# Optimization experiments

Hardware: AMD Instinct MI355X
Metric: run time of the kernel (lower is better)

Reference implementation:

```python
import jax, jax.numpy as jnp
import numpy as np

B, N = 4, 8192


def _nn_idx(a, b):
    # For each point in a [B,Na,3], index of nearest point in b [B,Nb,3].
    # ||a-b||^2 = ||a||^2 - 2 a.b + ||b||^2 ; ||a||^2 is constant per row -> drop it.
    d = jnp.sum(b * b, axis=-1)[:, None, :] - 2.0 * jnp.einsum('bnd,bmd->bnm', a, b)
    return jnp.argmin(d, axis=-1)  # [B, Na]


def _thickness(white, pial):
    # Mirrors compute_thickness_vector: white = inner, pial = outer.
    bix = jnp.arange(white.shape[0])[:, None]
    i1 = _nn_idx(white, pial)            # NN in pial for each white point
    inner_th = pial[bix, i1] - white     # [B, Nw, 3]
    i2 = _nn_idx(pial, white)            # NN in white for each pial point
    outer_th = pial - white[bix, i2]     # [B, Np, 3]
    return inner_th, outer_th


def _msn(a, b):
    # MeanSquaredNormLoss with w=None: mean over all points of sum((a-b)^2, -1)
    return jnp.mean(jnp.sum((a - b) ** 2, axis=-1))


def _sym(a, b, i_a, i_b):
    # SymmetricMeanSquaredNormLoss.forward (batch_size > 1 path, no weights)
    bix = jnp.arange(a.shape[0])[:, None]
    return 0.5 * (_msn(a, b[bix, i_a]) + _msn(a[bix, i_b], b))


def setup_inputs() -> dict:
    key = jax.random.key(0)
    ks = jax.random.split(key, 8)
    return {
        'pred_white': jax.random.normal(ks[0], (B, N, 3), jnp.float32),
        'pred_pial': jax.random.normal(ks[1], (B, N, 3), jnp.float32),
        'true_white': jax.random.normal(ks[2], (B, N, 3), jnp.float32),
        'true_pial': jax.random.normal(ks[3], (B, N, 3), jnp.float32),
        'i_pred_white': jax.random.randint(ks[4], (B, N), 0, N, jnp.int32),
        'i_true_white': jax.random.randint(ks[5], (B, N), 0, N, jnp.int32),
        'i_pred_pial': jax.random.randint(ks[6], (B, N), 0, N, jnp.int32),
        'i_true_pial': jax.random.randint(ks[7], (B, N), 0, N, jnp.int32),
    }


def reference(pred_white, pred_pial, true_white, true_pial,
              i_pred_white, i_true_white, i_pred_pial, i_true_pial):
    yp_inner, yp_outer = _thickness(pred_white, pred_pial)
    yt_inner, yt_outer = _thickness(true_white, true_pial)
    return (0.5 * _sym(yp_inner, yt_inner, i_pred_white, i_true_white)
            + 0.5 * _sym(yp_outer, yt_outer, i_pred_pial, i_true_pial))
```

## Files before the change

### kernel.cpp

```cpp
#include <hip/hip_runtime.h>
#include <math.h>

#define BATCH 4
#define NPTS 8192
#define BN (BATCH * NPTS)
#define NDIR 4
#define NZB (NDIR * BATCH)

#define QK 8
#define SPL 8
#define SLICE (NPTS / SPL)
#define SUBT 128
#define NSUB (SLICE / SUBT)
#define NSUB_TOT (NPTS / SUBT)


__device__ __forceinline__ void pick_ab(int z, const float* pw, const float* pp,
                                        const float* tw, const float* tp,
                                        const float** qa, const float** cb) {
  if (z == 0)      { *qa = pw; *cb = pp; }
  else if (z == 1) { *qa = pp; *cb = pw; }
  else if (z == 2) { *qa = tw; *cb = tp; }
  else             { *qa = tp; *cb = tw; }
}

__global__ __launch_bounds__(256) void nn_partial_kernel(
    const float* __restrict__ pw, const float* __restrict__ pp,
    const float* __restrict__ tw, const float* __restrict__ tp,
    float* __restrict__ part_d, int* __restrict__ part_t,
    double* __restrict__ acc) {
  __shared__ float4 sh[SLICE];

  const int zb = blockIdx.z;
  const int z = zb >> 2;
  const int b = zb & 3;
  const float* qa;
  const float* cb;
  pick_ab(z, pw, pp, tw, tp, &qa, &cb);

  const int tid = threadIdx.x;
  const int cslice = blockIdx.y * SLICE;
  const float* cbb = cb + (size_t)b * NPTS * 3;

  for (int m = tid; m < SLICE; m += 256) {
    const float* c = cbb + (size_t)(cslice + m) * 3;
    const float bx = c[0], by = c[1], bz = c[2];
    sh[m] = make_float4(bx, by, bz, fmaf(bx, bx, fmaf(by, by, bz * bz)));
  }
  if (tid == 0 && blockIdx.x == 0 && blockIdx.y == 0 && blockIdx.z == 0)
    *acc = 0.0;
  __syncthreads();

  const int qbase = blockIdx.x * (256 * QK);
  float qx[QK], qy[QK], qz[QK], dmin[QK];
  int tile[QK];
  #pragma unroll
  for (int k = 0; k < QK; ++k) {
    const int n = qbase + tid + k * 256;
    const float* q = qa + ((size_t)b * NPTS + n) * 3;
    qx[k] = -2.0f * q[0];
    qy[k] = -2.0f * q[1];
    qz[k] = -2.0f * q[2];
    dmin[k] = INFINITY;
    tile[k] = 0;
  }

  for (int sub = 0; sub < NSUB; ++sub) {
    float pre[QK];
    #pragma unroll
    for (int k = 0; k < QK; ++k) pre[k] = dmin[k];

    const int base = sub * SUBT;
    #pragma unroll 2
    for (int m = 0; m < SUBT; ++m) {
      const float4 c = sh[base + m];
      #pragma unroll
      for (int k = 0; k < QK; ++k) {
        const float d = fmaf(qx[k], c.x, fmaf(qy[k], c.y, fmaf(qz[k], c.z, c.w)));
        dmin[k] = fminf(dmin[k], d);
      }
    }
    const int g = blockIdx.y * NSUB + sub;
    #pragma unroll
    for (int k = 0; k < QK; ++k)
      if (dmin[k] < pre[k]) tile[k] = g;
  }

  #pragma unroll
  for (int k = 0; k < QK; ++k) {
    const int n = qbase + tid + k * 256;
    const size_t o = ((size_t)zb * NPTS + n) * SPL + blockIdx.y;
    part_d[o] = dmin[k];
    part_t[o] = tile[k];
  }
}

__global__ __launch_bounds__(256) void nn_resolve_kernel(
    const float* __restrict__ pw, const float* __restrict__ pp,
    const float* __restrict__ tw, const float* __restrict__ tp,
    const float* __restrict__ part_d, const int* __restrict__ part_t,
    int* __restrict__ idx_all) {
  const int gid = blockIdx.x * 256 + threadIdx.x;
  const int zb = gid >> 13;
  const int n = gid & (NPTS - 1);
  const int z = zb >> 2;
  const int b = zb & 3;
  const float* qa;
  const float* cb;
  pick_ab(z, pw, pp, tw, tp, &qa, &cb);

  const size_t o = (size_t)gid * SPL;
  float best_d = part_d[o];
  int best_t = part_t[o];
  #pragma unroll
  for (int s = 1; s < SPL; ++s) {
    const float d = part_d[o + s];
    if (d < best_d) { best_d = d; best_t = part_t[o + s]; }
  }

  const float* q = qa + ((size_t)b * NPTS + n) * 3;
  const float qx = -2.0f * q[0];
  const float qy = -2.0f * q[1];
  const float qz = -2.0f * q[2];
  const float* cbb = cb + (size_t)b * NPTS * 3;
  const int m0 = best_t * SUBT;

  int best_i = NPTS;
  #pragma unroll 4
  for (int m = 0; m < SUBT; ++m) {
    const float* c = cbb + (size_t)(m0 + m) * 3;
    const float bx = c[0], by = c[1], bz = c[2];
    const float b2 = fmaf(bx, bx, fmaf(by, by, bz * bz));
    const float d = fmaf(qx, bx, fmaf(qy, by, fmaf(qz, bz, b2)));
    if (d == best_d && (m0 + m) < best_i) best_i = m0 + m;
  }
  idx_all[gid] = best_i;
}

__device__ __forceinline__ float3 ld3(const float* __restrict__ p, int i) {
  const float* q = p + (size_t)i * 3;
  return make_float3(q[0], q[1], q[2]);
}

__device__ __forceinline__ float diff_nrm2(float3 a1, float3 a2, float3 b1, float3 b2) {
  const float x = (a1.x - a2.x) - (b1.x - b2.x);
  const float y = (a1.y - a2.y) - (b1.y - b2.y);
  const float z = (a1.z - a2.z) - (b1.z - b2.z);
  return fmaf(x, x, fmaf(y, y, z * z));
}

__global__ __launch_bounds__(256) void loss_kernel(
    const float* __restrict__ pw, const float* __restrict__ pp,
    const float* __restrict__ tw, const float* __restrict__ tp,
    const int* __restrict__ ipw, const int* __restrict__ itw,
    const int* __restrict__ ipp, const int* __restrict__ itp,
    const int* __restrict__ idx_all, double* __restrict__ acc) {
  const int gid = blockIdx.x * 256 + threadIdx.x;
  const int term = blockIdx.y;
  const int b = gid >> 13;
  const int n = gid & (NPTS - 1);
  const int base = b * NPTS;

  const float* PW = pw + (size_t)base * 3;
  const float* PP = pp + (size_t)base * 3;
  const float* TW = tw + (size_t)base * 3;
  const float* TP = tp + (size_t)base * 3;
  const int* I1P = idx_all + (0 * BATCH + b) * NPTS;
  const int* I2P = idx_all + (1 * BATCH + b) * NPTS;
  const int* I1T = idx_all + (2 * BATCH + b) * NPTS;
  const int* I2T = idx_all + (3 * BATCH + b) * NPTS;

  float s;
  if (term == 0) {
    const int j = ipw[base + n];
    s = diff_nrm2(ld3(PP, I1P[n]), ld3(PW, n), ld3(TP, I1T[j]), ld3(TW, j));
  } else if (term == 1) {
    const int k = itw[base + n];
    s = diff_nrm2(ld3(PP, I1P[k]), ld3(PW, k), ld3(TP, I1T[n]), ld3(TW, n));
  } else if (term == 2) {
    const int j = ipp[base + n];
    s = diff_nrm2(ld3(PP, n), ld3(PW, I2P[n]), ld3(TP, j), ld3(TW, I2T[j]));
  } else {
    const int k = itp[base + n];
    s = diff_nrm2(ld3(PP, k), ld3(PW, I2P[k]), ld3(TP, n), ld3(TW, I2T[n]));
  }

  double ds = (double)s;
  #pragma unroll
  for (int o = 32; o > 0; o >>= 1) ds += __shfl_down(ds, o, 64);
  if ((threadIdx.x & 63) == 0) atomicAdd(acc, ds);
}

__global__ void finalize_kernel(const double* __restrict__ acc,
                                float* __restrict__ out) {
  out[0] = (float)(0.25 * (*acc) / (double)BN);
}

extern "C" void kernel_launch(void* const* d_in, const int* in_sizes, int n_in,
                              void* d_out, int out_size, void* d_ws, size_t ws_size,
                              hipStream_t stream) {
  const float* pw = (const float*)d_in[0];
  const float* pp = (const float*)d_in[1];
  const float* tw = (const float*)d_in[2];
  const float* tp = (const float*)d_in[3];
  const int* ipw = (const int*)d_in[4];
  const int* itw = (const int*)d_in[5];
  const int* ipp = (const int*)d_in[6];
  const int* itp = (const int*)d_in[7];

  char* ws = (char*)d_ws;
  double* acc = (double*)ws;
  int* idx_all = (int*)(ws + 64);
  float* part_d = (float*)(ws + 64 + (size_t)NZB * NPTS * 4);
  int* part_t = (int*)(ws + 64 + (size_t)NZB * NPTS * 4 + (size_t)NZB * NPTS * SPL * 4);
  float* out = (float*)d_out;

  dim3 grid_nn(NPTS / (256 * QK), SPL, NZB);
  nn_partial_kernel<<<grid_nn, 256, 0, stream>>>(pw, pp, tw, tp, part_d, part_t, acc);

  nn_resolve_kernel<<<(NZB * NPTS) / 256, 256, 0, stream>>>(
      pw, pp, tw, tp, part_d, part_t, idx_all);

  dim3 grid_loss(BN / 256, 4);
  loss_kernel<<<grid_loss, 256, 0, stream>>>(pw, pp, tw, tp, ipw, itw, ipp, itp,
                                             idx_all, acc);

  finalize_kernel<<<1, 1, 0, stream>>>(acc, out);
}
```

Baseline: 213.1 us.

## Drop sub-tile tracking in NN scan, resolve argmin per slice with wavefront

The partial nearest-neighbour kernel no longer tracks which 128-point sub-tile produced the minimum. It only keeps the minimum distance per slice, processes two candidates per iteration, doubles the number of candidate slices, and stores partials in a slice-major layout. The resolve kernel now uses one 64-lane wavefront per query: it reduces the slice minima with shuffles, then rescans the whole winning slice in parallel to find the smallest matching index. This strips compare/select work from the hot inner loop and adds more blocks for occupancy, at the cost of a larger rescan in the resolve step. Zeroing of the accumulator also moves into the resolve kernel.

```diff
diff --git a/kernel.cpp b/kernel.cpp
--- a/kernel.cpp
+++ b/kernel.cpp
@@ -4,15 +4,11 @@
 #define BATCH 4
 #define NPTS 8192
 #define BN (BATCH * NPTS)
-#define NDIR 4
-#define NZB (NDIR * BATCH)
-
+#define NZB 16
 #define QK 8
-#define SPL 8
+#define SPL 16
 #define SLICE (NPTS / SPL)
-#define SUBT 128
-#define NSUB (SLICE / SUBT)
-#define NSUB_TOT (NPTS / SUBT)
+#define QBLK (256 * QK)
 
 
 __device__ __forceinline__ void pick_ab(int z, const float* pw, const float* pp,
@@ -24,11 +20,10 @@
   else             { *qa = tp; *cb = tw; }
 }
 
-__global__ __launch_bounds__(256) void nn_partial_kernel(
+__global__ __launch_bounds__(256, 4) void nn_partial_kernel(
     const float* __restrict__ pw, const float* __restrict__ pp,
     const float* __restrict__ tw, const float* __restrict__ tp,
-    float* __restrict__ part_d, int* __restrict__ part_t,
-    double* __restrict__ acc) {
+    float* __restrict__ part_d) {
   __shared__ float4 sh[SLICE];
 
   const int zb = blockIdx.z;
@@ -47,13 +42,10 @@
     const float bx = c[0], by = c[1], bz = c[2];
     sh[m] = make_float4(bx, by, bz, fmaf(bx, bx, fmaf(by, by, bz * bz)));
   }
-  if (tid == 0 && blockIdx.x == 0 && blockIdx.y == 0 && blockIdx.z == 0)
-    *acc = 0.0;
   __syncthreads();
 
-  const int qbase = blockIdx.x * (256 * QK);
+  const int qbase = blockIdx.x * QBLK;
   float qx[QK], qy[QK], qz[QK], dmin[QK];
-  int tile[QK];
   #pragma unroll
   for (int k = 0; k < QK; ++k) {
     const int n = qbase + tid + k * 256;
@@ -62,79 +54,81 @@
     qy[k] = -2.0f * q[1];
     qz[k] = -2.0f * q[2];
     dmin[k] = INFINITY;
-    tile[k] = 0;
-  }
-
-  for (int sub = 0; sub < NSUB; ++sub) {
-    float pre[QK];
-    #pragma unroll
-    for (int k = 0; k < QK; ++k) pre[k] = dmin[k];
-
-    const int base = sub * SUBT;
-    #pragma unroll 2
-    for (int m = 0; m < SUBT; ++m) {
-      const float4 c = sh[base + m];
-      #pragma unroll
-      for (int k = 0; k < QK; ++k) {
-        const float d = fmaf(qx[k], c.x, fmaf(qy[k], c.y, fmaf(qz[k], c.z, c.w)));
-        dmin[k] = fminf(dmin[k], d);
-      }
-    }
-    const int g = blockIdx.y * NSUB + sub;
+  }
+
+  #pragma unroll 2
+  for (int p = 0; p < SLICE / 2; ++p) {
+    const float4 c0 = sh[2 * p];
+    const float4 c1 = sh[2 * p + 1];
+    float t0[QK], t1[QK];
     #pragma unroll
     for (int k = 0; k < QK; ++k)
-      if (dmin[k] < pre[k]) tile[k] = g;
+      t0[k] = fmaf(qx[k], c0.x, fmaf(qy[k], c0.y, fmaf(qz[k], c0.z, c0.w)));
+    #pragma unroll
+    for (int k = 0; k < QK; ++k)
+      t1[k] = fmaf(qx[k], c1.x, fmaf(qy[k], c1.y, fmaf(qz[k], c1.z, c1.w)));
+    #pragma unroll
+    for (int k = 0; k < QK; ++k)
+      dmin[k] = fminf(fminf(t0[k], t1[k]), dmin[k]);
   }
 
   #pragma unroll
   for (int k = 0; k < QK; ++k) {
     const int n = qbase + tid + k * 256;
-    const size_t o = ((size_t)zb * NPTS + n) * SPL + blockIdx.y;
-    part_d[o] = dmin[k];
-    part_t[o] = tile[k];
-  }
-}
-
-__global__ __launch_bounds__(256) void nn_resolve_kernel(
+    part_d[(size_t)blockIdx.y * (NZB * NPTS) + (size_t)zb * NPTS + n] = dmin[k];
+  }
+}
+
+__global__ __launch_bounds__(1024) void nn_resolve_kernel(
     const float* __restrict__ pw, const float* __restrict__ pp,
     const float* __restrict__ tw, const float* __restrict__ tp,
-    const float* __restrict__ part_d, const int* __restrict__ part_t,
-    int* __restrict__ idx_all) {
-  const int gid = blockIdx.x * 256 + threadIdx.x;
-  const int zb = gid >> 13;
-  const int n = gid & (NPTS - 1);
+    const float* __restrict__ part_d, int* __restrict__ idx_all,
+    double* __restrict__ acc) {
+  if (blockIdx.x == 0 && threadIdx.x == 0) *acc = 0.0;
+
+  const int qid = (blockIdx.x * 1024 + threadIdx.x) >> 6;
+  const int lane = threadIdx.x & 63;
+  const int zb = qid >> 13;
+  const int n = qid & (NPTS - 1);
   const int z = zb >> 2;
   const int b = zb & 3;
   const float* qa;
   const float* cb;
   pick_ab(z, pw, pp, tw, tp, &qa, &cb);
 
-  const size_t o = (size_t)gid * SPL;
-  float best_d = part_d[o];
-  int best_t = part_t[o];
-  #pragma unroll
-  for (int s = 1; s < SPL; ++s) {
-    const float d = part_d[o + s];
-    if (d < best_d) { best_d = d; best_t = part_t[o + s]; }
-  }
+  float d = INFINITY;
+  int s = lane;
+  if (lane < SPL) d = part_d[(size_t)lane * (NZB * NPTS) + qid];
+  #pragma unroll
+  for (int off = 8; off > 0; off >>= 1) {
+    const float d2 = __shfl_down(d, off);
+    const int s2 = __shfl_down(s, off);
+    if (d2 < d || (d2 == d && s2 < s)) { d = d2; s = s2; }
+  }
+  const float best_d = __shfl(d, 0);
+  const int best_s = __shfl(s, 0);
 
   const float* q = qa + ((size_t)b * NPTS + n) * 3;
   const float qx = -2.0f * q[0];
   const float qy = -2.0f * q[1];
   const float qz = -2.0f * q[2];
   const float* cbb = cb + (size_t)b * NPTS * 3;
-  const int m0 = best_t * SUBT;
-
-  int best_i = NPTS;
-  #pragma unroll 4
-  for (int m = 0; m < SUBT; ++m) {
-    const float* c = cbb + (size_t)(m0 + m) * 3;
+  const int base = best_s * SLICE;
+
+  int best_i = 0x7fffffff;
+  #pragma unroll
+  for (int j = 0; j < SLICE / 64; ++j) {
+    const int m = base + lane * (SLICE / 64) + j;
+    const float* c = cbb + (size_t)m * 3;
     const float bx = c[0], by = c[1], bz = c[2];
     const float b2 = fmaf(bx, bx, fmaf(by, by, bz * bz));
-    const float d = fmaf(qx, bx, fmaf(qy, by, fmaf(qz, bz, b2)));
-    if (d == best_d && (m0 + m) < best_i) best_i = m0 + m;
-  }
-  idx_all[gid] = best_i;
+    const float dd = fmaf(qx, bx, fmaf(qy, by, fmaf(qz, bz, b2)));
+    if (dd == best_d) best_i = min(best_i, m);
+  }
+  #pragma unroll
+  for (int off = 32; off > 0; off >>= 1)
+    best_i = min(best_i, __shfl_down(best_i, off));
+  if (lane == 0) idx_all[qid] = best_i;
 }
 
 __device__ __forceinline__ float3 ld3(const float* __restrict__ p, int i) {
@@ -170,22 +164,22 @@
   const int* I1T = idx_all + (2 * BATCH + b) * NPTS;
   const int* I2T = idx_all + (3 * BATCH + b) * NPTS;
 
-  float s;
+  float sv;
   if (term == 0) {
     const int j = ipw[base + n];
-    s = diff_nrm2(ld3(PP, I1P[n]), ld3(PW, n), ld3(TP, I1T[j]), ld3(TW, j));
+    sv = diff_nrm2(ld3(PP, I1P[n]), ld3(PW, n), ld3(TP, I1T[j]), ld3(TW, j));
   } else if (term == 1) {
     const int k = itw[base + n];
-    s = diff_nrm2(ld3(PP, I1P[k]), ld3(PW, k), ld3(TP, I1T[n]), ld3(TW, n));
+    sv = diff_nrm2(ld3(PP, I1P[k]), ld3(PW, k), ld3(TP, I1T[n]), ld3(TW, n));
   } else if (term == 2) {
     const int j = ipp[base + n];
-    s = diff_nrm2(ld3(PP, n), ld3(PW, I2P[n]), ld3(TP, j), ld3(TW, I2T[j]));
+    sv = diff_nrm2(ld3(PP, n), ld3(PW, I2P[n]), ld3(TP, j), ld3(TW, I2T[j]));
   } else {
     const int k = itp[base + n];
-    s = diff_nrm2(ld3(PP, k), ld3(PW, I2P[k]), ld3(TP, n), ld3(TW, I2T[n]));
-  }
-
-  double ds = (double)s;
+    sv = diff_nrm2(ld3(PP, k), ld3(PW, I2P[k]), ld3(TP, n), ld3(TW, I2T[n]));
+  }
+
+  double ds = (double)sv;
   #pragma unroll
   for (int o = 32; o > 0; o >>= 1) ds += __shfl_down(ds, o, 64);
   if ((threadIdx.x & 63) == 0) atomicAdd(acc, ds);
@@ -212,14 +206,13 @@
   double* acc = (double*)ws;
   int* idx_all = (int*)(ws + 64);
   float* part_d = (float*)(ws + 64 + (size_t)NZB * NPTS * 4);
-  int* part_t = (int*)(ws + 64 + (size_t)NZB * NPTS * 4 + (size_t)NZB * NPTS * SPL * 4);
   float* out = (float*)d_out;
 
-  dim3 grid_nn(NPTS / (256 * QK), SPL, NZB);
-  nn_partial_kernel<<<grid_nn, 256, 0, stream>>>(pw, pp, tw, tp, part_d, part_t, acc);
-
-  nn_resolve_kernel<<<(NZB * NPTS) / 256, 256, 0, stream>>>(
-      pw, pp, tw, tp, part_d, part_t, idx_all);
+  dim3 grid_nn(NPTS / QBLK, SPL, NZB);
+  nn_partial_kernel<<<grid_nn, 256, 0, stream>>>(pw, pp, tw, tp, part_d);
+
+  nn_resolve_kernel<<<(NZB * NPTS) / 16, 1024, 0, stream>>>(
+      pw, pp, tw, tp, part_d, idx_all, acc);
 
   dim3 grid_loss(BN / 256, 4);
   loss_kernel<<<grid_loss, 256, 0, stream>>>(pw, pp, tw, tp, ipw, itw, ipp, itp,
```

After: 228.8 us. +7.4%, slower.
